# Kernel tuning notes

Hardware: AMD Instinct MI355X
Metric: run time of the kernel (lower is better)

The kernel has to match this reference:

```python
import jax, jax.numpy as jnp
import numpy as np

B, L, C = 8, 256, 64
NEG = -1e30  # large negative instead of -inf to keep grads NaN-free


def setup_inputs() -> dict:
    key = jax.random.key(0)
    k1, k2 = jax.random.split(key)
    scores = jax.random.normal(k1, (B, L, L, C), dtype=jnp.float32)
    lens = jax.random.randint(k2, (B,), 64, L, dtype=jnp.int32)  # sentence lengths in [64, L-1]
    return {"scores": scores, "lens": lens}


def _inside_max(scores, lens):
    """Max-semiring CKY inside pass. scores: [B,L,L,C]; returns logZ per batch [B]."""
    t = jnp.transpose(jnp.max(scores, axis=-1), (1, 2, 0))  # [L,L,B] best label per span
    s0 = jnp.zeros((L, L, B), scores.dtype)                 # chart s[i,j] = best score of span (i,j)
    i = jnp.arange(L)
    j = jnp.arange(L)

    def step(s, w):
        e = jnp.clip(i + w, 0, L - 1)                       # span end, [L]
        k = jnp.clip(i[:, None] + j[None, :], 0, L - 1)     # split points, [L,L]
        left = s[i[:, None], k]                             # s[i, i+j], [L,L,B]
        right = s[k, e[:, None]]                            # s[i+j, i+w], [L,L,B]
        valid = (j[None, :] >= 1) & (j[None, :] < w) & ((i + w) < L)[:, None]
        comb = jnp.max(jnp.where(valid[..., None], left + right, NEG), axis=1)  # [L,B]
        s_l = t[i, e]                                       # label-max span score, [L,B]
        diag = jnp.where(w == 1, s_l, comb + s_l)
        row_ok = ((i + w) < L)[:, None]
        upd = jnp.where(row_ok, diag, s[i, e])
        s = s.at[i, e].set(upd)
        return s, None

    s, _ = jax.lax.scan(step, s0, jnp.arange(1, L))
    lens_c = jnp.clip(lens, 1, L - 1)
    return s[0, lens_c, jnp.arange(B)]                      # logZ (best tree score) per sentence


def reference(scores, lens):
    return _inside_max(scores, lens)
```

## Files before the change

kernel.cpp:

```cpp
#include <hip/hip_runtime.h>

#define LVAL 256
#define T    32
#define ST   36
#define SLAB (T * ST)
#define NB   8
#define NEG  (-1e30f)

typedef float f32x4 __attribute__((ext_vector_type(4)));

#define SOFT_FENCE() asm volatile("" ::: "memory")

__device__ __forceinline__ size_t sidx(int b, int i, int e) {
    return ((size_t)b << 16) + (i << 8) + e;
}

__device__ __forceinline__ void st_coh4(float* p, f32x4 v) {
    asm volatile("global_store_dwordx4 %0, %1, off sc0 sc1"
                 :: "v"(p), "v"(v) : "memory");
}
__device__ __forceinline__ f32x4 ld_coh4(const float* p) {
    f32x4 v;
    asm volatile("global_load_dwordx4 %0, %1, off sc0 sc1\n\t"
                 "s_waitcnt vmcnt(0)"
                 : "=&v"(v) : "v"(p) : "memory");
    return v;
}
__device__ __forceinline__ void ld_coh4x4(const float* p,
                                          f32x4& a, f32x4& b, f32x4& c, f32x4& d) {
    asm volatile("global_load_dwordx4 %0, %4, off sc0 sc1\n\t"
                 "global_load_dwordx4 %1, %4, off offset:16 sc0 sc1\n\t"
                 "global_load_dwordx4 %2, %4, off offset:32 sc0 sc1\n\t"
                 "global_load_dwordx4 %3, %4, off offset:48 sc0 sc1\n\t"
                 "s_waitcnt vmcnt(0)"
                 : "=&v"(a), "=&v"(b), "=&v"(c), "=&v"(d)
                 : "v"(p) : "memory");
}
__device__ __forceinline__ void st_coh1(int* p, int v) {
    asm volatile("global_store_dword %0, %1, off sc0 sc1"
                 :: "v"(p), "v"(v) : "memory");
}
__device__ __forceinline__ int ld_coh1(const int* p) {
    int v;
    asm volatile("global_load_dword %0, %1, off sc0 sc1\n\t"
                 "s_waitcnt vmcnt(0)"
                 : "=&v"(v) : "v"(p) : "memory");
    return v;
}
__device__ __forceinline__ void spin_flag(int* f) {
    int guard = 0;
    while (ld_coh1(f) == 0) {
        if (++guard > (1 << 20)) break;
    }
}

template<int CTRL>
__device__ __forceinline__ float dpp_max(float v) {
#if __has_builtin(__builtin_amdgcn_mov_dpp)
    int o = __builtin_amdgcn_mov_dpp(__builtin_bit_cast(int, v), CTRL, 0xF, 0xF, true);
    return fmaxf(v, __builtin_bit_cast(float, o));
#else
    return fmaxf(v, __shfl_xor(v, CTRL == 0xB1 ? 1 : 2));
#endif
}

__global__ __launch_bounds__(256) void phase1(const float* __restrict__ scores,
                                              float* __restrict__ s,
                                              int* __restrict__ bar) {
    if (blockIdx.x == 0 && blockIdx.y == 0) {
        for (int k = threadIdx.x; k < 2048; k += 256) bar[k] = 0;
    }
    const int i = blockIdx.x, b = blockIdx.y;
    const int sub = threadIdx.x & 15, slot = threadIdx.x >> 4;
    const float* row = scores + ((((size_t)b * LVAL + i) * LVAL) << 6);
    #pragma unroll 4
    for (int m0 = 0; m0 < LVAL; m0 += 16) {
        const int e = m0 + slot;
        if (e > i) {
            float4 v = *((const float4*)(row + ((size_t)e << 6)) + sub);
            float mx = fmaxf(fmaxf(v.x, v.y), fmaxf(v.z, v.w));
            #pragma unroll
            for (int d = 1; d < 16; d <<= 1) mx = fmaxf(mx, __shfl_xor(mx, d));
            if (sub == 0) s[sidx(b, i, e)] = mx;
        }
    }
}

template<int LP>
__device__ __forceinline__ void diag_step(int lane, int l,
                                          float (*cur)[ST], float (*curT)[ST],
                                          const float (*tb)[ST]) {
    const int cells = T - l;
    const int P = 1 << LP;
    const int c = lane >> LP, p = lane & (P - 1);
    const bool guard = c < cells;
    const int li = guard ? c : 0;
    const int le = guard ? c + l : 0;
    constexpr int NF = 8 >> LP;
    const float tv = tb[li][le];
    float acc = NEG;
    #pragma unroll
    for (int m = 0; m < NF; ++m) {
        const int k0 = 4 * (p + m * P);
        float4 cu = *(const float4*)&cur[li][k0];
        float4 ct = *(const float4*)&curT[le][k0];
        acc = fmaxf(acc, fmaxf(fmaxf(cu.x + ct.x, cu.y + ct.y),
                               fmaxf(cu.z + ct.z, cu.w + ct.w)));
    }
    acc = dpp_max<0xB1>(acc);
    if (LP >= 2) acc = dpp_max<0x4E>(acc);
    const float v = acc + tv;
    if (guard && p == 0) cur[li][le] = v;
    if (guard && p == 1) curT[le][li] = v;
}

template<int LP>
__device__ __forceinline__ void edge_step(int lane, int l, int D,
                                          const float (*Ae)[ST], const float (*BeT)[ST],
                                          float (*cur)[ST], float (*curT)[ST],
                                          const float (*tb)[ST], const float (*pre)[ST]) {
    const int delta = l - (T - 1);
    const int ad = delta < 0 ? -delta : delta;
    const int cells = T - ad;
    const int P = 1 << LP;
    const int c = lane >> LP, p = lane & (P - 1);
    const bool guard = c < cells;
    const int li = guard ? (delta < 0 ? c + ad : c) : 0;
    const int le = guard ? li + delta : 0;
    constexpr int NF = 8 >> LP;
    const float tv = tb[li][le];
    float acc = pre[li][le];
    #pragma unroll
    for (int m = 0; m < NF; ++m) {
        const int k0 = 4 * (p + m * P);
        float4 a  = *(const float4*)&Ae[li][k0];
        float4 ct = *(const float4*)&curT[le][k0];
        float4 cu = *(const float4*)&cur[li][k0];
        float4 bt = *(const float4*)&BeT[le][k0];
        float s0 = fmaxf(fmaxf(a.x + ct.x, a.y + ct.y), fmaxf(a.z + ct.z, a.w + ct.w));
        float s1 = fmaxf(fmaxf(cu.x + bt.x, cu.y + bt.y), fmaxf(cu.z + bt.z, cu.w + bt.w));
        acc = fmaxf(acc, fmaxf(s0, s1));
    }
    acc = dpp_max<0xB1>(acc);
    if (LP >= 2) acc = dpp_max<0x4E>(acc);
    const float v = (D == 1 && l == 0) ? tv : acc + tv;
    if (guard && p == 0) cur[li][le] = v;
    if (guard && p == 1) curT[le][li] = v;
}

__device__ __forceinline__ void gemm_blk(const float* ATs, const float (*BW)[ST],
                                         int r0, int c0, float (&ag)[4][4]) {
    const float (*AT)[ST] = (const float(*)[ST])ATs;
    #pragma unroll 4
    for (int k = 0; k < T; ++k) {
        f32x4 a4 = *(const f32x4*)&AT[k][r0];
        f32x4 b4 = *(const f32x4*)&BW[k][c0];
        #pragma unroll
        for (int i = 0; i < 4; ++i)
            #pragma unroll
            for (int j = 0; j < 4; ++j)
                ag[i][j] = fmaxf(ag[i][j], a4[i] + b4[j]);
    }
}

__global__ __launch_bounds__(256) void dp_fused(float* __restrict__ s,
                                                const int* __restrict__ lens,
                                                float* __restrict__ out,
                                                int* __restrict__ bar) {
    __shared__ __align__(16) float smem[14 * SLAB];
    float* ATb = smem;
    float (*Ae)[ST]  = (float(*)[ST])(smem + 6 * SLAB);
    float (*tb)[ST]  = (float(*)[ST])(smem + 7 * SLAB);
    float (*BeT)[ST] = (float(*)[ST])(smem + 8 * SLAB);
    float (*cur)[ST] = (float(*)[ST])(smem + 9 * SLAB);
    float* BWb = smem + 10 * SLAB;
    float (*pre)[ST] = (float(*)[ST])BWb;

    const int b  = blockIdx.x & 7;
    const int bi = blockIdx.x >> 3;
    const int tid = threadIdx.x, wid = tid >> 6, lane = tid & 63;
    const int lr = tid >> 5, lc = tid & 31;
    const int grow = lane >> 1, gc = (lane & 1) * 16;
    const int gly = lane >> 3, glx = lane & 7, r0 = 4 * gly, c0 = 4 * glx;
    const int trow = tid >> 3, tc4 = (tid & 7) * 4;
    float (*BW)[ST] = (float(*)[ST])(BWb + wid * SLAB);
    int* flags = bar + b * 64;

    f32x4 tpb[4], bpb[4];

    if (wid == 0) {
        float (*curT0)[ST] = (float(*)[ST])(BWb + 1 * SLAB);
        float (*t0)[ST]    = (float(*)[ST])(BWb + 2 * SLAB);
        const float4 negv = make_float4(NEG, NEG, NEG, NEG);
        #pragma unroll
        for (int j = 0; j < 4; ++j) {
            float4 v = *(const float4*)&s[sidx(b, bi * T + grow, bi * T + gc + 4 * j)];
            *(float4*)&t0[grow][gc + 4 * j]    = v;
            *(float4*)&Ae[grow][gc + 4 * j]    = negv;
            *(float4*)&curT0[grow][gc + 4 * j] = negv;
        }
        SOFT_FENCE();
        if (lane < T - 1) {
            float v = t0[lane][lane + 1];
            Ae[lane][lane + 1] = v;
            curT0[lane + 1][lane] = v;
        }
        SOFT_FENCE();
        #pragma unroll 1
        for (int l = 2; l < T; ++l) {
            if (T - l <= 16) diag_step<2>(lane, l, Ae, curT0, t0);
            else             diag_step<1>(lane, l, Ae, curT0, t0);
            SOFT_FENCE();
        }
        #pragma unroll
        for (int j = 0; j < 4; ++j)
            st_coh4(&s[sidx(b, bi * T + grow, bi * T + gc + 4 * j)],
                    *(const f32x4*)&Ae[grow][gc + 4 * j]);
        asm volatile("s_waitcnt vmcnt(0)" ::: "memory");
        if (lane == 0) st_coh1(&flags[bi * 8 + bi], 1);
    } else if (bi + 1 < NB) {
        for (int idx = tid - 64; idx < 256; idx += 192) {
            const int row = idx >> 3, c4 = (idx & 7) * 4;
            *(float4*)&tb[row][c4] =
                *(const float4*)&s[sidx(b, bi * T + row, (bi + 1) * T + c4)];
        }
    }

    #pragma unroll 1
    for (int D = 1; D <= NB - 1 - bi; ++D) {
        const int be = bi + D;
        if (tid == 0) {
            for (int K = bi + 1; K < be; ++K) spin_flag(&flags[K * 8 + be]);
            if (D == 1) spin_flag(&flags[be * 8 + be]);
        }
        __syncthreads();
        if (D == 1) {
            f32x4 v = ld_coh4(&s[sidx(b, be * T + trow, be * T + tc4)]);
            BeT[tc4 + 0][trow] = (trow < tc4 + 0) ? v[0] : NEG;
            BeT[tc4 + 1][trow] = (trow < tc4 + 1) ? v[1] : NEG;
            BeT[tc4 + 2][trow] = (trow < tc4 + 2) ? v[2] : NEG;
            BeT[tc4 + 3][trow] = (trow < tc4 + 3) ? v[3] : NEG;
        }
        const int nw = (D - 1 < 4) ? (D - 1) : 4;
        float ag[4][4];
        #pragma unroll
        for (int i = 0; i < 4; ++i)
            #pragma unroll
            for (int j = 0; j < 4; ++j) ag[i][j] = NEG;
        for (int K = bi + 1 + wid; K < be; K += 4) {
            const float (*AT)[ST] = (const float(*)[ST])(ATb + (K - bi - 1) * SLAB);
            f32x4 b0, b1, b2, b3;
            ld_coh4x4(&s[sidx(b, K * T + grow, be * T + gc)], b0, b1, b2, b3);
            *(f32x4*)&BW[grow][gc + 0]  = b0;
            *(f32x4*)&BW[grow][gc + 4]  = b1;
            *(f32x4*)&BW[grow][gc + 8]  = b2;
            *(f32x4*)&BW[grow][gc + 12] = b3;
            SOFT_FENCE();
            gemm_blk((const float*)AT, BW, r0, c0, ag);
            SOFT_FENCE();
        }
        if (wid < nw) {
            #pragma unroll
            for (int i = 0; i < 4; ++i)
                *(f32x4*)&BW[r0 + i][c0] =
                    f32x4{ag[i][0], ag[i][1], ag[i][2], ag[i][3]};
        }
        __syncthreads();
        #pragma unroll
        for (int r = 0; r < 4; ++r) {
            const int row = lr + 8 * r;
            float v = NEG;
            for (int w2 = 0; w2 < nw; ++w2)
                v = fmaxf(v, BWb[w2 * SLAB + row * ST + lc]);
            pre[row][lc] = v;
        }
        __syncthreads();
        float (*curT)[ST] = (D == NB - 1) ? (float(*)[ST])(BWb + 1 * SLAB)
                                          : (float(*)[ST])(ATb + (D - 1) * SLAB);
        #pragma unroll
        for (int r = 0; r < 4; ++r) {
            const int row = lr + 8 * r;
            cur[row][lc]  = NEG;
            curT[row][lc] = NEG;
        }
        __syncthreads();
        if (wid == 0) {
            #pragma unroll 1
            for (int l = 0; l < 2 * T - 1; ++l) {
                const int ad0 = (l < T - 1) ? (T - 1 - l) : (l - (T - 1));
                if (ad0 >= 16) edge_step<2>(lane, l, D, Ae, BeT, cur, curT, tb, pre);
                else           edge_step<1>(lane, l, D, Ae, BeT, cur, curT, tb, pre);
                SOFT_FENCE();
            }
        } else if (be + 1 < NB) {
            if (wid == 1) {
                #pragma unroll
                for (int j = 0; j < 4; ++j)
                    tpb[j] = *(const f32x4*)&s[sidx(b, bi * T + grow,
                                                    (be + 1) * T + gc + 4 * j)];
            }
            if (wid == 2) {
                spin_flag(&flags[(be + 1) * 8 + (be + 1)]);
                #pragma unroll
                for (int j = 0; j < 4; ++j)
                    bpb[j] = ld_coh4(&s[sidx(b, (be + 1) * T + grow,
                                             (be + 1) * T + gc + 4 * j)]);
            }
        }
        __syncthreads();
        {
            f32x4 pv = *(const f32x4*)&cur[trow][tc4];
            st_coh4(&s[sidx(b, bi * T + trow, be * T + tc4)], pv);
        }
        asm volatile("s_waitcnt vmcnt(0)" ::: "memory");
        __syncthreads();
        if (tid == 0) st_coh1(&flags[bi * 8 + be], 1);
        if (be + 1 < NB) {
            if (wid == 1) {
                #pragma unroll
                for (int j = 0; j < 4; ++j)
                    *(f32x4*)&tb[grow][gc + 4 * j] = tpb[j];
            }
            if (wid == 2) {
                #pragma unroll
                for (int j = 0; j < 4; ++j)
                    #pragma unroll
                    for (int k = 0; k < 4; ++k) {
                        const int col = gc + 4 * j + k;
                        BeT[col][grow] = (grow < col) ? bpb[j][k] : NEG;
                    }
            }
        }
    }

    if (bi == 0 && tid == 0) {
        int len = lens[b];
        len = len < 1 ? 1 : (len > LVAL - 1 ? LVAL - 1 : len);
        const int K = len >> 5, off = len & 31;
        float r;
        if (K == 0)           r = Ae[0][off];
        else if (K == NB - 1) r = cur[0][off];
        else                  r = ATb[(K - 1) * SLAB + off * ST];
        out[b] = r;
    }
}

extern "C" void kernel_launch(void* const* d_in, const int* in_sizes, int n_in,
                              void* d_out, int out_size, void* d_ws, size_t ws_size,
                              hipStream_t stream) {
    const float* scores = (const float*)d_in[0];
    const int*   lens   = (const int*)d_in[1];
    float*       out    = (float*)d_out;
    float*       s      = (float*)d_ws;
    int*         bar    = (int*)((char*)d_ws + ((size_t)(8) << 16) * sizeof(float));

    phase1<<<dim3(LVAL, 8), 256, 0, stream>>>(scores, s, bar);
    dp_fused<<<64, 256, 0, stream>>>(s, lens, out, bar);
}
```

Before: 339.1 us.

## Spread diagonal DP steps across all four wavefronts and batch coherent loads

The in-tile diagonal and edge DP sweeps now use all 256 threads, eight lanes per cell, instead of a single wavefront. Each step ends with a block-wide __syncthreads rather than a wave-local fence. The removed per-wave prefetch of the next tile's data is replaced by issuing all coherent global loads for a tile up front without per-load waits, followed by one vmcnt wait. This trades more barriers per step for more parallel lanes and fewer serialized load round-trips, and it removes the overlap of next-tile prefetch with the edge sweep.

```diff
diff --git a/kernel.cpp b/kernel.cpp
--- a/kernel.cpp
+++ b/kernel.cpp
@@ -19,22 +19,11 @@
     asm volatile("global_store_dwordx4 %0, %1, off sc0 sc1"
                  :: "v"(p), "v"(v) : "memory");
 }
-__device__ __forceinline__ f32x4 ld_coh4(const float* p) {
+__device__ __forceinline__ f32x4 ld_coh4_nw(const float* p) {
     f32x4 v;
-    asm volatile("global_load_dwordx4 %0, %1, off sc0 sc1\n\t"
-                 "s_waitcnt vmcnt(0)"
+    asm volatile("global_load_dwordx4 %0, %1, off sc0 sc1"
                  : "=&v"(v) : "v"(p) : "memory");
     return v;
-}
-__device__ __forceinline__ void ld_coh4x4(const float* p,
-                                          f32x4& a, f32x4& b, f32x4& c, f32x4& d) {
-    asm volatile("global_load_dwordx4 %0, %4, off sc0 sc1\n\t"
-                 "global_load_dwordx4 %1, %4, off offset:16 sc0 sc1\n\t"
-                 "global_load_dwordx4 %2, %4, off offset:32 sc0 sc1\n\t"
-                 "global_load_dwordx4 %3, %4, off offset:48 sc0 sc1\n\t"
-                 "s_waitcnt vmcnt(0)"
-                 : "=&v"(a), "=&v"(b), "=&v"(c), "=&v"(d)
-                 : "v"(p) : "memory");
 }
 __device__ __forceinline__ void st_coh1(int* p, int v) {
     asm volatile("global_store_dword %0, %1, off sc0 sc1"
@@ -62,6 +51,20 @@
 #else
     return fmaxf(v, __shfl_xor(v, CTRL == 0xB1 ? 1 : 2));
 #endif
+}
+__device__ __forceinline__ float dpp_max_shl4(float v) {
+#if __has_builtin(__builtin_amdgcn_mov_dpp)
+    int o = __builtin_amdgcn_mov_dpp(__builtin_bit_cast(int, v), 0x104, 0xF, 0xF, true);
+    return fmaxf(v, __builtin_bit_cast(float, o));
+#else
+    return fmaxf(v, __shfl_xor(v, 4));
+#endif
+}
+
+__device__ __forceinline__ float red4(const f32x4 a, const f32x4 b) {
+    float m0 = fmaxf(a.x + b.x, a.y + b.y);
+    float m1 = fmaxf(a.z + b.z, a.w + b.w);
+    return fmaxf(m0, m1);
 }
 
 __global__ __launch_bounds__(256) void phase1(const float* __restrict__ scores,
@@ -86,66 +89,54 @@
     }
 }
 
-template<int LP>
-__device__ __forceinline__ void diag_step(int lane, int l,
-                                          float (*cur)[ST], float (*curT)[ST],
-                                          const float (*tb)[ST]) {
+__device__ __forceinline__ void diag_step8(int tid, int l,
+        float (*cur0)[ST], float (*curT0)[ST], const float (*t0)[ST]) {
     const int cells = T - l;
-    const int P = 1 << LP;
-    const int c = lane >> LP, p = lane & (P - 1);
-    const bool guard = c < cells;
-    const int li = guard ? c : 0;
-    const int le = guard ? c + l : 0;
-    constexpr int NF = 8 >> LP;
-    const float tv = tb[li][le];
-    float acc = NEG;
-    #pragma unroll
-    for (int m = 0; m < NF; ++m) {
-        const int k0 = 4 * (p + m * P);
-        float4 cu = *(const float4*)&cur[li][k0];
-        float4 ct = *(const float4*)&curT[le][k0];
-        acc = fmaxf(acc, fmaxf(fmaxf(cu.x + ct.x, cu.y + ct.y),
-                               fmaxf(cu.z + ct.z, cu.w + ct.w)));
-    }
+    const int oct = tid >> 3, q = tid & 7;
+    const bool g = oct < cells;
+    const int li = g ? oct : 0;
+    const int le = g ? oct + l : 0;
+    const int k0 = q * 4;
+    f32x4 x = *(const f32x4*)&cur0[li][k0];
+    f32x4 y = *(const f32x4*)&curT0[le][k0];
+    const float tv = t0[li][le];
+    float acc = red4(x, y);
     acc = dpp_max<0xB1>(acc);
-    if (LP >= 2) acc = dpp_max<0x4E>(acc);
+    acc = dpp_max<0x4E>(acc);
+    acc = dpp_max_shl4(acc);
     const float v = acc + tv;
-    if (guard && p == 0) cur[li][le] = v;
-    if (guard && p == 1) curT[le][li] = v;
-}
-
-template<int LP>
-__device__ __forceinline__ void edge_step(int lane, int l, int D,
-                                          const float (*Ae)[ST], const float (*BeT)[ST],
-                                          float (*cur)[ST], float (*curT)[ST],
-                                          const float (*tb)[ST], const float (*pre)[ST]) {
+    if (g && q == 0) cur0[li][le] = v;
+    if (g && q == 1) curT0[le][li] = v;
+}
+
+__device__ __forceinline__ void edge_step8(int tid, int l, int D,
+        const float (*Ae)[ST], const float (*BeT)[ST],
+        float (*cur)[ST], float (*curT)[ST],
+        const float (*tb)[ST], const float (*pre)[ST]) {
     const int delta = l - (T - 1);
     const int ad = delta < 0 ? -delta : delta;
     const int cells = T - ad;
-    const int P = 1 << LP;
-    const int c = lane >> LP, p = lane & (P - 1);
-    const bool guard = c < cells;
-    const int li = guard ? (delta < 0 ? c + ad : c) : 0;
-    const int le = guard ? li + delta : 0;
-    constexpr int NF = 8 >> LP;
+    const int oct = tid >> 3, q = tid & 7;
+    const bool g = oct < cells;
+    const int li = g ? (delta < 0 ? oct + ad : oct) : 0;
+    const int le = g ? li + delta : 0;
+    const int k0 = (q & 3) * 8;
+    const float* r1 = (q < 4) ? &Ae[li][0]   : &cur[li][0];
+    const float* r2 = (q < 4) ? &curT[le][0] : &BeT[le][0];
+    f32x4 x0 = *(const f32x4*)&r1[k0];
+    f32x4 y0 = *(const f32x4*)&r2[k0];
+    f32x4 x1 = *(const f32x4*)&r1[k0 + 4];
+    f32x4 y1 = *(const f32x4*)&r2[k0 + 4];
     const float tv = tb[li][le];
-    float acc = pre[li][le];
-    #pragma unroll
-    for (int m = 0; m < NF; ++m) {
-        const int k0 = 4 * (p + m * P);
-        float4 a  = *(const float4*)&Ae[li][k0];
-        float4 ct = *(const float4*)&curT[le][k0];
-        float4 cu = *(const float4*)&cur[li][k0];
-        float4 bt = *(const float4*)&BeT[le][k0];
-        float s0 = fmaxf(fmaxf(a.x + ct.x, a.y + ct.y), fmaxf(a.z + ct.z, a.w + ct.w));
-        float s1 = fmaxf(fmaxf(cu.x + bt.x, cu.y + bt.y), fmaxf(cu.z + bt.z, cu.w + bt.w));
-        acc = fmaxf(acc, fmaxf(s0, s1));
-    }
-    acc = dpp_max<0xB1>(acc);
-    if (LP >= 2) acc = dpp_max<0x4E>(acc);
+    const float pr = pre[li][le];
+    float local = fmaxf(red4(x0, y0), red4(x1, y1));
+    local = fmaxf(local, pr);
+    float acc = dpp_max<0xB1>(local);
+    acc = dpp_max<0x4E>(acc);
+    acc = dpp_max_shl4(acc);
     const float v = (D == 1 && l == 0) ? tv : acc + tv;
-    if (guard && p == 0) cur[li][le] = v;
-    if (guard && p == 1) curT[le][li] = v;
+    if (g && q == 0) cur[li][le] = v;
+    if (g && q == 1) curT[le][li] = v;
 }
 
 __device__ __forceinline__ void gemm_blk(const float* ATs, const float (*BW)[ST],
@@ -186,78 +177,88 @@
     float (*BW)[ST] = (float(*)[ST])(BWb + wid * SLAB);
     int* flags = bar + b * 64;
 
-    f32x4 tpb[4], bpb[4];
-
-    if (wid == 0) {
+    {
         float (*curT0)[ST] = (float(*)[ST])(BWb + 1 * SLAB);
         float (*t0)[ST]    = (float(*)[ST])(BWb + 2 * SLAB);
-        const float4 negv = make_float4(NEG, NEG, NEG, NEG);
-        #pragma unroll
-        for (int j = 0; j < 4; ++j) {
-            float4 v = *(const float4*)&s[sidx(b, bi * T + grow, bi * T + gc + 4 * j)];
-            *(float4*)&t0[grow][gc + 4 * j]    = v;
-            *(float4*)&Ae[grow][gc + 4 * j]    = negv;
-            *(float4*)&curT0[grow][gc + 4 * j] = negv;
-        }
-        SOFT_FENCE();
-        if (lane < T - 1) {
-            float v = t0[lane][lane + 1];
-            Ae[lane][lane + 1] = v;
-            curT0[lane + 1][lane] = v;
-        }
-        SOFT_FENCE();
+        const f32x4 negv = {NEG, NEG, NEG, NEG};
+        f32x4 v = *(const f32x4*)&s[sidx(b, bi * T + trow, bi * T + tc4)];
+        *(f32x4*)&t0[trow][tc4]    = v;
+        *(f32x4*)&Ae[trow][tc4]    = negv;
+        *(f32x4*)&curT0[trow][tc4] = negv;
+        if (bi + 1 < NB) {
+            f32x4 w = *(const f32x4*)&s[sidx(b, bi * T + trow, (bi + 1) * T + tc4)];
+            *(f32x4*)&tb[trow][tc4] = w;
+        }
+        __syncthreads();
+        if (tid < T - 1) {
+            float d = t0[tid][tid + 1];
+            Ae[tid][tid + 1] = d;
+            curT0[tid + 1][tid] = d;
+        }
+        __syncthreads();
         #pragma unroll 1
         for (int l = 2; l < T; ++l) {
-            if (T - l <= 16) diag_step<2>(lane, l, Ae, curT0, t0);
-            else             diag_step<1>(lane, l, Ae, curT0, t0);
-            SOFT_FENCE();
-        }
-        #pragma unroll
-        for (int j = 0; j < 4; ++j)
-            st_coh4(&s[sidx(b, bi * T + grow, bi * T + gc + 4 * j)],
-                    *(const f32x4*)&Ae[grow][gc + 4 * j]);
+            diag_step8(tid, l, Ae, curT0, t0);
+            __syncthreads();
+        }
+        st_coh4(&s[sidx(b, bi * T + trow, bi * T + tc4)],
+                *(const f32x4*)&Ae[trow][tc4]);
         asm volatile("s_waitcnt vmcnt(0)" ::: "memory");
-        if (lane == 0) st_coh1(&flags[bi * 8 + bi], 1);
-    } else if (bi + 1 < NB) {
-        for (int idx = tid - 64; idx < 256; idx += 192) {
-            const int row = idx >> 3, c4 = (idx & 7) * 4;
-            *(float4*)&tb[row][c4] =
-                *(const float4*)&s[sidx(b, bi * T + row, (bi + 1) * T + c4)];
-        }
+        __syncthreads();
+        if (tid == 0) st_coh1(&flags[bi * 8 + bi], 1);
     }
 
     #pragma unroll 1
     for (int D = 1; D <= NB - 1 - bi; ++D) {
         const int be = bi + D;
         if (tid == 0) {
-            for (int K = bi + 1; K < be; ++K) spin_flag(&flags[K * 8 + be]);
-            if (D == 1) spin_flag(&flags[be * 8 + be]);
-        }
-        __syncthreads();
-        if (D == 1) {
-            f32x4 v = ld_coh4(&s[sidx(b, be * T + trow, be * T + tc4)]);
-            BeT[tc4 + 0][trow] = (trow < tc4 + 0) ? v[0] : NEG;
-            BeT[tc4 + 1][trow] = (trow < tc4 + 1) ? v[1] : NEG;
-            BeT[tc4 + 2][trow] = (trow < tc4 + 2) ? v[2] : NEG;
-            BeT[tc4 + 3][trow] = (trow < tc4 + 3) ? v[3] : NEG;
-        }
+            spin_flag(&flags[be * 8 + be]);
+            for (int K = be - 1; K >= bi + 1; --K) spin_flag(&flags[K * 8 + be]);
+        }
+        __syncthreads();
+        f32x4 dg = ld_coh4_nw(&s[sidx(b, be * T + trow, be * T + tc4)]);
+        f32x4 tbv = *(const f32x4*)&s[sidx(b, bi * T + trow, be * T + tc4)];
+        const int KA = bi + 1 + wid, KB = bi + 5 + wid;
+        const bool hA = (KA < be), hB = (KB < be);
+        f32x4 a0, a1, a2, a3, bb0, bb1, bb2, bb3;
+        if (hA) {
+            const float* p = &s[sidx(b, KA * T + grow, be * T + gc)];
+            a0 = ld_coh4_nw(p);     a1 = ld_coh4_nw(p + 4);
+            a2 = ld_coh4_nw(p + 8); a3 = ld_coh4_nw(p + 12);
+        }
+        if (hB) {
+            const float* p = &s[sidx(b, KB * T + grow, be * T + gc)];
+            bb0 = ld_coh4_nw(p);     bb1 = ld_coh4_nw(p + 4);
+            bb2 = ld_coh4_nw(p + 8); bb3 = ld_coh4_nw(p + 12);
+        }
+        asm volatile("s_waitcnt vmcnt(0)" ::: "memory");
+        BeT[tc4 + 0][trow] = (trow < tc4 + 0) ? dg[0] : NEG;
+        BeT[tc4 + 1][trow] = (trow < tc4 + 1) ? dg[1] : NEG;
+        BeT[tc4 + 2][trow] = (trow < tc4 + 2) ? dg[2] : NEG;
+        BeT[tc4 + 3][trow] = (trow < tc4 + 3) ? dg[3] : NEG;
+        *(f32x4*)&tb[trow][tc4] = tbv;
         const int nw = (D - 1 < 4) ? (D - 1) : 4;
         float ag[4][4];
         #pragma unroll
         for (int i = 0; i < 4; ++i)
             #pragma unroll
             for (int j = 0; j < 4; ++j) ag[i][j] = NEG;
-        for (int K = bi + 1 + wid; K < be; K += 4) {
-            const float (*AT)[ST] = (const float(*)[ST])(ATb + (K - bi - 1) * SLAB);
-            f32x4 b0, b1, b2, b3;
-            ld_coh4x4(&s[sidx(b, K * T + grow, be * T + gc)], b0, b1, b2, b3);
-            *(f32x4*)&BW[grow][gc + 0]  = b0;
-            *(f32x4*)&BW[grow][gc + 4]  = b1;
-            *(f32x4*)&BW[grow][gc + 8]  = b2;
-            *(f32x4*)&BW[grow][gc + 12] = b3;
+        if (hA) {
+            *(f32x4*)&BW[grow][gc + 0]  = a0;
+            *(f32x4*)&BW[grow][gc + 4]  = a1;
+            *(f32x4*)&BW[grow][gc + 8]  = a2;
+            *(f32x4*)&BW[grow][gc + 12] = a3;
             SOFT_FENCE();
-            gemm_blk((const float*)AT, BW, r0, c0, ag);
+            gemm_blk(ATb + wid * SLAB, BW, r0, c0, ag);
             SOFT_FENCE();
+        }
+        if (hB) {
+            *(f32x4*)&BW[grow][gc + 0]  = bb0;
+            *(f32x4*)&BW[grow][gc + 4]  = bb1;
+            *(f32x4*)&BW[grow][gc + 8]  = bb2;
+            *(f32x4*)&BW[grow][gc + 12] = bb3;
+            SOFT_FENCE();
+            gemm_blk(ATb + (wid + 4) * SLAB, BW, r0, c0, ag);
         }
         if (wid < nw) {
             #pragma unroll
@@ -284,30 +285,11 @@
             curT[row][lc] = NEG;
         }
         __syncthreads();
-        if (wid == 0) {
-            #pragma unroll 1
-            for (int l = 0; l < 2 * T - 1; ++l) {
-                const int ad0 = (l < T - 1) ? (T - 1 - l) : (l - (T - 1));
-                if (ad0 >= 16) edge_step<2>(lane, l, D, Ae, BeT, cur, curT, tb, pre);
-                else           edge_step<1>(lane, l, D, Ae, BeT, cur, curT, tb, pre);
-                SOFT_FENCE();
-            }
-        } else if (be + 1 < NB) {
-            if (wid == 1) {
-                #pragma unroll
-                for (int j = 0; j < 4; ++j)
-                    tpb[j] = *(const f32x4*)&s[sidx(b, bi * T + grow,
-                                                    (be + 1) * T + gc + 4 * j)];
-            }
-            if (wid == 2) {
-                spin_flag(&flags[(be + 1) * 8 + (be + 1)]);
-                #pragma unroll
-                for (int j = 0; j < 4; ++j)
-                    bpb[j] = ld_coh4(&s[sidx(b, (be + 1) * T + grow,
-                                             (be + 1) * T + gc + 4 * j)]);
-            }
-        }
-        __syncthreads();
+        #pragma unroll 1
+        for (int l = 0; l < 2 * T - 1; ++l) {
+            edge_step8(tid, l, D, Ae, BeT, cur, curT, tb, pre);
+            __syncthreads();
+        }
         {
             f32x4 pv = *(const f32x4*)&cur[trow][tc4];
             st_coh4(&s[sidx(b, bi * T + trow, be * T + tc4)], pv);
@@ -315,22 +297,6 @@
         asm volatile("s_waitcnt vmcnt(0)" ::: "memory");
         __syncthreads();
         if (tid == 0) st_coh1(&flags[bi * 8 + be], 1);
-        if (be + 1 < NB) {
-            if (wid == 1) {
-                #pragma unroll
-                for (int j = 0; j < 4; ++j)
-                    *(f32x4*)&tb[grow][gc + 4 * j] = tpb[j];
-            }
-            if (wid == 2) {
-                #pragma unroll
-                for (int j = 0; j < 4; ++j)
-                    #pragma unroll
-                    for (int k = 0; k < 4; ++k) {
-                        const int col = gc + 4 * j + k;
-                        BeT[col][grow] = (grow < col) ? bpb[j][k] : NEG;
-                    }
-            }
-        }
     }
 
     if (bi == 0 && tid == 0) {
```

Measured after the change: 342.1 us. No clear change (+0.9%).

## Software-pipeline diagonal edge steps with register exchange of fresh neighbor cells

Applied to the files above, without the earlier changes.

The serial 63-step anti-diagonal loop in the block-edge solver now prefetches the next diagonal's LDS operands while the current one is computed. The dependency on the just-written neighbouring diagonal is served through DPP row shifts and readlane instead of LDS, so the prefetch can safely run ahead. The per-step width is fixed at 2 lanes per cell. Flag spin order is also changed so the diagonal-block flag is checked first. This adds register pressure and lane-exchange logic that must exactly match the cell-to-lane mapping at boundaries.

```diff
diff --git a/kernel.cpp b/kernel.cpp
--- a/kernel.cpp
+++ b/kernel.cpp
@@ -10,6 +10,11 @@
 typedef float f32x4 __attribute__((ext_vector_type(4)));
 
 #define SOFT_FENCE() asm volatile("" ::: "memory")
+#if __has_builtin(__builtin_amdgcn_sched_barrier)
+#define SCHED_FENCE() __builtin_amdgcn_sched_barrier(0)
+#else
+#define SCHED_FENCE() SOFT_FENCE()
+#endif
 
 __device__ __forceinline__ size_t sidx(int b, int i, int e) {
     return ((size_t)b << 16) + (i << 8) + e;
@@ -62,6 +67,53 @@
 #else
     return fmaxf(v, __shfl_xor(v, CTRL == 0xB1 ? 1 : 2));
 #endif
+}
+
+__device__ __forceinline__ float exch_vn(float vprev, int c, bool dpos) {
+#if __has_builtin(__builtin_amdgcn_mov_dpp) && __has_builtin(__builtin_amdgcn_readlane)
+    if (dpos) {
+        int o = __builtin_amdgcn_mov_dpp(__builtin_bit_cast(int, vprev),
+                                         0x102, 0xF, 0xF, true);
+        float vn = __builtin_bit_cast(float, o);
+        float s0 = __builtin_bit_cast(float,
+            __builtin_amdgcn_readlane(__builtin_bit_cast(int, vprev), 16));
+        float s1 = __builtin_bit_cast(float,
+            __builtin_amdgcn_readlane(__builtin_bit_cast(int, vprev), 32));
+        float s2 = __builtin_bit_cast(float,
+            __builtin_amdgcn_readlane(__builtin_bit_cast(int, vprev), 48));
+        if (c == 7)  vn = s0;
+        if (c == 15) vn = s1;
+        if (c == 23) vn = s2;
+        if (c == 31) vn = NEG;
+        return vn;
+    } else {
+        int o = __builtin_amdgcn_mov_dpp(__builtin_bit_cast(int, vprev),
+                                         0x112, 0xF, 0xF, true);
+        float vn = __builtin_bit_cast(float, o);
+        float s0 = __builtin_bit_cast(float,
+            __builtin_amdgcn_readlane(__builtin_bit_cast(int, vprev), 14));
+        float s1 = __builtin_bit_cast(float,
+            __builtin_amdgcn_readlane(__builtin_bit_cast(int, vprev), 30));
+        float s2 = __builtin_bit_cast(float,
+            __builtin_amdgcn_readlane(__builtin_bit_cast(int, vprev), 46));
+        if (c == 8)  vn = s0;
+        if (c == 16) vn = s1;
+        if (c == 24) vn = s2;
+        if (c == 0)  vn = NEG;
+        return vn;
+    }
+#else
+    return __shfl(vprev, (int)(threadIdx.x & 63) + (dpos ? 2 : -2));
+#endif
+}
+
+__device__ __forceinline__ float red8(const f32x4 a, const f32x4 b,
+                                      const f32x4 c, const f32x4 d) {
+    float m0 = fmaxf(a.x + b.x, a.y + b.y);
+    float m1 = fmaxf(a.z + b.z, a.w + b.w);
+    float m2 = fmaxf(c.x + d.x, c.y + d.y);
+    float m3 = fmaxf(c.z + d.z, c.w + d.w);
+    return fmaxf(fmaxf(m0, m1), fmaxf(m2, m3));
 }
 
 __global__ __launch_bounds__(256) void phase1(const float* __restrict__ scores,
@@ -114,38 +166,62 @@
     if (guard && p == 1) curT[le][li] = v;
 }
 
-template<int LP>
-__device__ __forceinline__ void edge_step(int lane, int l, int D,
-                                          const float (*Ae)[ST], const float (*BeT)[ST],
-                                          float (*cur)[ST], float (*curT)[ST],
-                                          const float (*tb)[ST], const float (*pre)[ST]) {
+struct EC {
+    f32x4 a[4], ct[4], cu[4], bt[4];
+    float tv, pr, afr, bfr;
+};
+
+__device__ __forceinline__ EC eprefetch(int l, int c, int p,
+        const float (*Ae)[ST], const float (*BeT)[ST],
+        const float (*cur)[ST], const float (*curT)[ST],
+        const float (*tb)[ST], const float (*pre)[ST]) {
+    EC e;
     const int delta = l - (T - 1);
     const int ad = delta < 0 ? -delta : delta;
     const int cells = T - ad;
-    const int P = 1 << LP;
-    const int c = lane >> LP, p = lane & (P - 1);
-    const bool guard = c < cells;
-    const int li = guard ? (delta < 0 ? c + ad : c) : 0;
-    const int le = guard ? li + delta : 0;
-    constexpr int NF = 8 >> LP;
-    const float tv = tb[li][le];
-    float acc = pre[li][le];
+    const bool g = c < cells;
+    const int li = g ? (delta < 0 ? c + ad : c) : 0;
+    const int le = g ? li + delta : 0;
+    e.tv  = tb[li][le];
+    e.pr  = pre[li][le];
+    e.afr = Ae[li][li + 1];
+    e.bfr = BeT[le][le > 0 ? le - 1 : 0];
     #pragma unroll
-    for (int m = 0; m < NF; ++m) {
-        const int k0 = 4 * (p + m * P);
-        float4 a  = *(const float4*)&Ae[li][k0];
-        float4 ct = *(const float4*)&curT[le][k0];
-        float4 cu = *(const float4*)&cur[li][k0];
-        float4 bt = *(const float4*)&BeT[le][k0];
-        float s0 = fmaxf(fmaxf(a.x + ct.x, a.y + ct.y), fmaxf(a.z + ct.z, a.w + ct.w));
-        float s1 = fmaxf(fmaxf(cu.x + bt.x, cu.y + bt.y), fmaxf(cu.z + bt.z, cu.w + bt.w));
-        acc = fmaxf(acc, fmaxf(s0, s1));
-    }
+    for (int m = 0; m < 4; ++m) {
+        const int k0 = 4 * (p + 2 * m);
+        e.a[m]  = *(const f32x4*)&Ae[li][k0];
+        e.ct[m] = *(const f32x4*)&curT[le][k0];
+        e.cu[m] = *(const f32x4*)&cur[li][k0];
+        e.bt[m] = *(const f32x4*)&BeT[le][k0];
+    }
+    return e;
+}
+
+__device__ __forceinline__ float ecompute(int l, int c, int p, int D,
+        const EC& e, float vprev, float vn,
+        float (*cur)[ST], float (*curT)[ST]) {
+    const int delta = l - (T - 1);
+    const int ad = delta < 0 ? -delta : delta;
+    const int cells = T - ad;
+    const bool g = c < cells;
+    const int li = g ? (delta < 0 ? c + ad : c) : 0;
+    const int le = g ? li + delta : 0;
+    const bool dpos = delta > 0;
+    float acc = e.pr;
+    #pragma unroll
+    for (int m = 0; m < 4; ++m)
+        acc = fmaxf(acc, red8(e.a[m], e.ct[m], e.cu[m], e.bt[m]));
+    const float srcL = dpos ? vn : vprev;
+    const float srcR = dpos ? vprev : vn;
+    const bool okL = dpos || (c != cells - 1);
+    const bool okR = dpos || (c != 0);
+    acc = fmaxf(acc, okL ? e.afr + srcL : NEG);
+    acc = fmaxf(acc, okR ? srcR + e.bfr : NEG);
     acc = dpp_max<0xB1>(acc);
-    if (LP >= 2) acc = dpp_max<0x4E>(acc);
-    const float v = (D == 1 && l == 0) ? tv : acc + tv;
-    if (guard && p == 0) cur[li][le] = v;
-    if (guard && p == 1) curT[le][li] = v;
+    const float v = (D == 1 && l == 0) ? e.tv : acc + e.tv;
+    if (g && p == 0) cur[li][le] = v;
+    if (g && p == 1) curT[le][li] = v;
+    return g ? v : NEG;
 }
 
 __device__ __forceinline__ void gemm_blk(const float* ATs, const float (*BW)[ST],
@@ -230,8 +306,8 @@
     for (int D = 1; D <= NB - 1 - bi; ++D) {
         const int be = bi + D;
         if (tid == 0) {
-            for (int K = bi + 1; K < be; ++K) spin_flag(&flags[K * 8 + be]);
-            if (D == 1) spin_flag(&flags[be * 8 + be]);
+            spin_flag(&flags[be * 8 + be]);
+            for (int K = be - 1; K >= bi + 1; --K) spin_flag(&flags[K * 8 + be]);
         }
         __syncthreads();
         if (D == 1) {
@@ -285,12 +361,28 @@
         }
         __syncthreads();
         if (wid == 0) {
+            const int c = lane >> 1, p = lane & 1;
+            EC fA = eprefetch(0, c, p, Ae, BeT, cur, curT, tb, pre);
+            EC fB;
+            float vprev = NEG;
+            SOFT_FENCE();
             #pragma unroll 1
-            for (int l = 0; l < 2 * T - 1; ++l) {
-                const int ad0 = (l < T - 1) ? (T - 1 - l) : (l - (T - 1));
-                if (ad0 >= 16) edge_step<2>(lane, l, D, Ae, BeT, cur, curT, tb, pre);
-                else           edge_step<1>(lane, l, D, Ae, BeT, cur, curT, tb, pre);
-                SOFT_FENCE();
+            for (int l = 0; l < 2 * T; l += 2) {
+                {
+                    float vn = exch_vn(vprev, c, l > T - 1);
+                    fB = eprefetch(l + 1, c, p, Ae, BeT, cur, curT, tb, pre);
+                    SCHED_FENCE();
+                    vprev = ecompute(l, c, p, D, fA, vprev, vn, cur, curT);
+                    SOFT_FENCE();
+                }
+                {
+                    float vn = exch_vn(vprev, c, l + 1 > T - 1);
+                    if (l + 2 < 2 * T)
+                        fA = eprefetch(l + 2, c, p, Ae, BeT, cur, curT, tb, pre);
+                    SCHED_FENCE();
+                    vprev = ecompute(l + 1, c, p, D, fB, vprev, vn, cur, curT);
+                    SOFT_FENCE();
+                }
             }
         } else if (be + 1 < NB) {
             if (wid == 1) {
```

Measured after the change: 374.6 us. +10.5%, slower.
